# Performance work log

Hardware: AMD Instinct MI355X
Metric: run time of the kernel (lower is better)

The kernel has to match this reference:

```python
import jax, jax.numpy as jnp
import numpy as np

B, D, L, E, H = 8192, 1024, 256, 16, 400

def setup_inputs() -> dict:
    key = jax.random.key(0)
    ks = jax.random.split(key, 6)
    s1 = 1.0 / np.sqrt(D)
    s2 = 1.0 / np.sqrt(H)
    return {
        "x": jax.random.normal(ks[0], (B, D), dtype=jnp.float32),
        "angle_idx": jax.random.randint(ks[1], (B,), 0, E, dtype=jnp.int64),
        "W1": jax.random.uniform(ks[2], (E, D, H), jnp.float32, -s1, s1),
        "b1": jax.random.uniform(ks[3], (E, H), jnp.float32, -s1, s1),
        "W2": jax.random.uniform(ks[4], (E, H, 2 * L), jnp.float32, -s2, s2),
        "b2": jax.random.uniform(ks[5], (E, 2 * L), jnp.float32, -s2, s2),
    }

def reference(x, angle_idx, W1, b1, W2, b2):
    # Dense all-experts compute, then per-sample select (jit-friendly MoE dispatch).
    # h1: [E, B, H]
    h1 = jax.nn.relu(jnp.einsum('bd,edh->ebh', x, W1) + b1[:, None, :])
    # h: [E, B, 2L]
    h = jnp.einsum('ebh,ehk->ebk', h1, W2) + b2[:, None, :]
    sel = h[angle_idx, jnp.arange(x.shape[0])]  # [B, 2L], each row from its routed expert
    half = sel.shape[1] // 2
    z_mu, z_logvar = sel[:, :half], sel[:, half:]
    return (z_mu, z_logvar)
```

## Files before the change

kernel.cpp:

```cpp
#include <hip/hip_runtime.h>
#include <hip/hip_bf16.h>
#include <cstdint>
#include <cstddef>

#define B_N 8192
#define D_K 1024
#define H_N 400
#define HP  416
#define K2_N 512
#define E_N 16
#define L_N 256
#define TM 64
#define PAD_ROWS (B_N + E_N * TM)
#define NTILES (PAD_ROWS / TM)

typedef short bf16x8 __attribute__((ext_vector_type(8)));
typedef float f32x4 __attribute__((ext_vector_type(4)));

#define GLDS(gp, lp) __builtin_amdgcn_global_load_lds( \
    (const __attribute__((address_space(1))) unsigned int*)(gp), \
    (__attribute__((address_space(3))) unsigned int*)(lp), 16, 0, 0)

static __device__ __forceinline__ unsigned short f2bf(float f) {
  union { float f; unsigned int u; } c; c.f = f;
  unsigned int u = c.u + 0x7fffu + ((c.u >> 16) & 1u);
  return (unsigned short)(u >> 16);
}
static __device__ __forceinline__ unsigned int pkbf(float a, float b) {
  union { __hip_bfloat162 v; unsigned int u; } c;
  c.v = __float22bfloat162_rn(make_float2(a, b));
  return c.u;
}

__global__ __launch_bounds__(256) void prep_kernel(const float* __restrict__ W1,
                                                   const float* __restrict__ W2,
                                                   const int* __restrict__ idx,
                                                   unsigned short* __restrict__ Wt1,
                                                   unsigned short* __restrict__ Wt2,
                                                   int* __restrict__ off_al,
                                                   int* __restrict__ order) {
  const int bid = blockIdx.x;
  const int t = threadIdx.x;
  if (bid < 2688) {
    __shared__ unsigned short Ls[64][72];
    const float* S; unsigned short* Dt; int K, N, Kd, Nd, k0, n0;
    if (bid < 1792) {
      int e = bid / 112, r = bid % 112;
      k0 = (r % 16) * 64; n0 = (r / 16) * 64;
      S = W1 + (size_t)e * D_K * H_N; Dt = Wt1 + (size_t)e * HP * D_K;
      K = D_K; N = H_N; Kd = D_K; Nd = HP;
    } else {
      int t2 = bid - 1792; int e = t2 / 56, r = t2 % 56;
      k0 = (r % 7) * 64; n0 = (r / 7) * 64;
      S = W2 + (size_t)e * H_N * K2_N; Dt = Wt2 + (size_t)e * K2_N * HP;
      K = H_N; N = K2_N; Kd = HP; Nd = K2_N;
    }
    const int kk = t >> 4;
    const int nn = (t & 15) * 4;
#pragma unroll
    for (int p = 0; p < 4; ++p) {
      int k = k0 + p * 16 + kk;
      int n = n0 + nn;
      float4 v = make_float4(0.f, 0.f, 0.f, 0.f);
      if (k < K && n + 3 < N) v = *(const float4*)(S + (size_t)k * N + n);
      Ls[nn + 0][p * 16 + kk] = f2bf(v.x);
      Ls[nn + 1][p * 16 + kk] = f2bf(v.y);
      Ls[nn + 2][p * 16 + kk] = f2bf(v.z);
      Ls[nn + 3][p * 16 + kk] = f2bf(v.w);
    }
    __syncthreads();
    const int n2 = t >> 3;
    const int ch = t & 7;
#pragma unroll
    for (int p = 0; p < 2; ++p) {
      int n = n0 + p * 32 + n2;
      int k = k0 + ch * 8;
      if (n < Nd && k < Kd)
        *(uint4*)(Dt + (size_t)n * Kd + k) = *(const uint4*)&Ls[p * 32 + n2][ch * 8];
    }
  } else {
    __shared__ int cnt[E_N];
    __shared__ int curS[E_N];
    if (t < E_N) cnt[t] = 0;
    __syncthreads();
    for (int b = t; b < B_N; b += 256) atomicAdd(&cnt[idx[b]], 1);
    __syncthreads();
    if (t == 0) {
      int acc = 0;
      for (int e = 0; e < E_N; ++e) {
        off_al[e] = acc; curS[e] = acc;
        acc += ((cnt[e] + TM - 1) / TM) * TM;
      }
      off_al[E_N] = acc;
    }
    for (int i = t; i < PAD_ROWS; i += 256) order[i] = -1;
    __syncthreads();
    for (int b = t; b < B_N; b += 256) {
      int e = idx[b];
      order[atomicAdd(&curS[e], 1)] = b;
    }
  }
}

__global__ __launch_bounds__(256) void gather_x_kernel(const float* __restrict__ x,
                                                       const int* __restrict__ order,
                                                       unsigned short* __restrict__ xg) {
  const int w = threadIdx.x >> 6, l = threadIdx.x & 63;
  const int row = blockIdx.x * 4 + w;
  const int src = order[row];
  unsigned short* dst = xg + (size_t)row * D_K;
  if (src < 0) {
#pragma unroll
    for (int i = 0; i < 4; ++i)
      *(uint2*)(dst + i * 256 + l * 4) = make_uint2(0, 0);
  } else {
    const float* s = x + (size_t)src * D_K;
#pragma unroll
    for (int i = 0; i < 4; ++i) {
      float4 v = *(const float4*)(s + i * 256 + l * 4);
      uint2 o; o.x = pkbf(v.x, v.y); o.y = pkbf(v.z, v.w);
      *(uint2*)(dst + i * 256 + l * 4) = o;
    }
  }
}

__global__ __launch_bounds__(256) void gemm1_kernel(const unsigned short* __restrict__ xg,
                                                    const unsigned short* __restrict__ Wt1,
                                                    const float* __restrict__ b1,
                                                    const int* __restrict__ off_al,
                                                    unsigned short* __restrict__ h1buf) {
  __shared__ unsigned short As[2][64 * 32];
  __shared__ unsigned short Bs[2][112 * 32];
  __shared__ int offs[E_N + 1];
  const int tid = threadIdx.x;
  const int m0 = blockIdx.x * TM;
  const int nb = blockIdx.y;
  const int tstart = (nb < 2) ? 7 * nb : 14 + 6 * (nb - 2);
  const int tcnt   = (nb < 2) ? 7 : 6;
  if (tid <= E_N) offs[tid] = off_al[tid];
  __syncthreads();
  if (m0 >= offs[E_N]) return;
  int e = 0;
  while (m0 >= offs[e + 1]) ++e;
  const unsigned short* Wt1e = Wt1 + (size_t)e * HP * D_K;

  const int l = tid & 63, w = tid >> 6;
  const int r4 = l >> 2;
  const int sg = (r4 ^ (r4 >> 2)) & 3;
  const int g8 = ((l & 3) ^ sg) * 8;
  const int tl1 = w + 4;
  const unsigned short* gA  = xg + (size_t)(m0 + 16 * w + r4) * D_K + g8;
  const unsigned short* gB0 = Wt1e + (size_t)((tstart + w) * 16 + r4) * D_K + g8;
  const unsigned short* gB1 = Wt1e + (size_t)((tstart + tl1) * 16 + r4) * D_K + g8;

  const int ln = l & 15, q = l >> 4;
  const int sr = (ln ^ (ln >> 2)) & 3;
  const int cq = (q ^ sr) * 8;

  f32x4 acc[4][2] = {};

  GLDS(gA, &As[0][16 * w * 32]);
  GLDS(gB0, &Bs[0][16 * w * 32]);
  if (tl1 < tcnt) GLDS(gB1, &Bs[0][16 * tl1 * 32]);

  for (int k0 = 0; k0 < D_K; k0 += 32) {
    const int cur = (k0 >> 5) & 1;
    const int nxt = cur ^ 1;
    __syncthreads();
    if (k0 + 32 < D_K) {
      GLDS(gA + k0 + 32, &As[nxt][16 * w * 32]);
      GLDS(gB0 + k0 + 32, &Bs[nxt][16 * w * 32]);
      if (tl1 < tcnt) GLDS(gB1 + k0 + 32, &Bs[nxt][16 * tl1 * 32]);
    }
    bf16x8 af[4];
#pragma unroll
    for (int i = 0; i < 4; ++i)
      af[i] = *(const bf16x8*)&As[cur][(16 * i + ln) * 32 + cq];
    {
      bf16x8 bf0 = *(const bf16x8*)&Bs[cur][(16 * w + ln) * 32 + cq];
#pragma unroll
      for (int i = 0; i < 4; ++i)
        acc[i][0] = __builtin_amdgcn_mfma_f32_16x16x32_bf16(af[i], bf0, acc[i][0], 0, 0, 0);
    }
    if (tl1 < tcnt) {
      bf16x8 bf1 = *(const bf16x8*)&Bs[cur][(16 * tl1 + ln) * 32 + cq];
#pragma unroll
      for (int i = 0; i < 4; ++i)
        acc[i][1] = __builtin_amdgcn_mfma_f32_16x16x32_bf16(af[i], bf1, acc[i][1], 0, 0, 0);
    }
  }

#pragma unroll
  for (int t = 0; t < 2; ++t) {
    const int tl = w + 4 * t;
    if (tl < tcnt) {
      const int n = (tstart + tl) * 16 + ln;
      if (n < H_N) {
        const float bias = b1[e * H_N + n];
#pragma unroll
        for (int i = 0; i < 4; ++i)
#pragma unroll
          for (int r = 0; r < 4; ++r) {
            const int m = m0 + 16 * i + 4 * q + r;
            h1buf[(size_t)m * HP + n] = f2bf(fmaxf(acc[i][t][r] + bias, 0.f));
          }
      }
    }
  }
  if (nb == 3 && tid < TM) {
    uint4 z = make_uint4(0, 0, 0, 0);
    *(uint4*)&h1buf[(size_t)(m0 + tid) * HP + 400] = z;
    *(uint4*)&h1buf[(size_t)(m0 + tid) * HP + 408] = z;
  }
}

__global__ __launch_bounds__(256) void gemm2_kernel(const unsigned short* __restrict__ h1buf,
                                                    const unsigned short* __restrict__ Wt2,
                                                    const float* __restrict__ b2,
                                                    const int* __restrict__ off_al,
                                                    const int* __restrict__ order,
                                                    float* __restrict__ out) {
  __shared__ unsigned short As[2][64 * 32];
  __shared__ unsigned short Bs[2][128 * 32];
  __shared__ int offs[E_N + 1];
  __shared__ int rowidx[TM];
  const int tid = threadIdx.x;
  const int m0 = blockIdx.x * TM;
  const int nbase = blockIdx.y * 128;
  if (tid <= E_N) offs[tid] = off_al[tid];
  if (tid < TM) rowidx[tid] = order[m0 + tid];
  __syncthreads();
  if (m0 >= offs[E_N]) return;
  int e = 0;
  while (m0 >= offs[e + 1]) ++e;
  const unsigned short* Wt2e = Wt2 + (size_t)e * K2_N * HP;

  const int l = tid & 63, w = tid >> 6;
  const int r4 = l >> 2;
  const int sg = (r4 ^ (r4 >> 2)) & 3;
  const int g8 = ((l & 3) ^ sg) * 8;
  const int tl1 = w + 4;
  const unsigned short* gA  = h1buf + (size_t)(m0 + 16 * w + r4) * HP + g8;
  const unsigned short* gB0 = Wt2e + (size_t)(nbase + 16 * w + r4) * HP + g8;
  const unsigned short* gB1 = Wt2e + (size_t)(nbase + 16 * tl1 + r4) * HP + g8;

  const int ln = l & 15, q = l >> 4;
  const int sr = (ln ^ (ln >> 2)) & 3;
  const int cq = (q ^ sr) * 8;

  f32x4 acc[4][2] = {};

  GLDS(gA, &As[0][16 * w * 32]);
  GLDS(gB0, &Bs[0][16 * w * 32]);
  GLDS(gB1, &Bs[0][16 * tl1 * 32]);

  for (int k0 = 0; k0 < HP; k0 += 32) {
    const int cur = (k0 >> 5) & 1;
    const int nxt = cur ^ 1;
    __syncthreads();
    if (k0 + 32 < HP) {
      GLDS(gA + k0 + 32, &As[nxt][16 * w * 32]);
      GLDS(gB0 + k0 + 32, &Bs[nxt][16 * w * 32]);
      GLDS(gB1 + k0 + 32, &Bs[nxt][16 * tl1 * 32]);
    }
    bf16x8 af[4];
#pragma unroll
    for (int i = 0; i < 4; ++i)
      af[i] = *(const bf16x8*)&As[cur][(16 * i + ln) * 32 + cq];
#pragma unroll
    for (int t = 0; t < 2; ++t) {
      const int tl = w + 4 * t;
      bf16x8 bfr = *(const bf16x8*)&Bs[cur][(16 * tl + ln) * 32 + cq];
#pragma unroll
      for (int i = 0; i < 4; ++i)
        acc[i][t] = __builtin_amdgcn_mfma_f32_16x16x32_bf16(af[i], bfr, acc[i][t], 0, 0, 0);
    }
  }

#pragma unroll
  for (int t = 0; t < 2; ++t) {
    const int tl = w + 4 * t;
    const int n = nbase + 16 * tl + ln;
    const float bias = b2[e * K2_N + n];
#pragma unroll
    for (int i = 0; i < 4; ++i)
#pragma unroll
      for (int r = 0; r < 4; ++r) {
        const int s = rowidx[16 * i + 4 * q + r];
        if (s >= 0) {
          const float v = acc[i][t][r] + bias;
          if (n < L_N) out[(size_t)s * L_N + n] = v;
          else         out[(size_t)(B_N + s) * L_N + (n - L_N)] = v;
        }
      }
  }
}

extern "C" void kernel_launch(void* const* d_in, const int* in_sizes, int n_in,
                              void* d_out, int out_size, void* d_ws, size_t ws_size,
                              hipStream_t stream) {
  const float* x   = (const float*)d_in[0];
  const int*   idx = (const int*)d_in[1];
  const float* W1  = (const float*)d_in[2];
  const float* b1  = (const float*)d_in[3];
  const float* W2  = (const float*)d_in[4];
  const float* b2  = (const float*)d_in[5];
  float* out = (float*)d_out;

  char* ws = (char*)d_ws;
  int* off_al = (int*)(ws + 0);
  int* order  = (int*)(ws + 2240);
  unsigned short* xg  = (unsigned short*)(ws + 39104);
  unsigned short* h1  = (unsigned short*)(ws + 18913472);
  unsigned short* Wt1 = (unsigned short*)(ws + 26581184);
  unsigned short* Wt2 = (unsigned short*)(ws + 40212672);

  prep_kernel<<<2689, 256, 0, stream>>>(W1, W2, idx, Wt1, Wt2, off_al, order);
  gather_x_kernel<<<PAD_ROWS / 4, 256, 0, stream>>>(x, order, xg);
  gemm1_kernel<<<dim3(NTILES, 4), 256, 0, stream>>>(xg, Wt1, b1, off_al, h1);
  gemm2_kernel<<<dim3(NTILES, 4), 256, 0, stream>>>(h1, Wt2, b2, off_al, order, out);
}
```

Before: 179.3 us.

## Fold x bf16 conversion into prep kernel and gather rows inside GEMM1

Removes the separate gather_x kernel. The prep kernel now converts x to bf16 in its original row order and adds one zero row at the end. GEMM1 then gathers A rows indirectly through the order array, with padding rows pointing at the zero row. This drops a kernel launch and a full write and re-read of the permuted activation buffer. The cost is indirect, non-contiguous row addressing for the A loads in GEMM1.

Measured after the change: 175.4 us. 1.02x faster.

```diff
diff --git a/kernel.cpp b/kernel.cpp
--- a/kernel.cpp
+++ b/kernel.cpp
@@ -34,9 +34,11 @@
 
 __global__ __launch_bounds__(256) void prep_kernel(const float* __restrict__ W1,
                                                    const float* __restrict__ W2,
+                                                   const float* __restrict__ x,
                                                    const int* __restrict__ idx,
                                                    unsigned short* __restrict__ Wt1,
                                                    unsigned short* __restrict__ Wt2,
+                                                   unsigned short* __restrict__ xc,
                                                    int* __restrict__ off_al,
                                                    int* __restrict__ order) {
   const int bid = blockIdx.x;
@@ -78,9 +80,20 @@
       if (n < Nd && k < Kd)
         *(uint4*)(Dt + (size_t)n * Kd + k) = *(const uint4*)&Ls[p * 32 + n2][ch * 8];
     }
+  } else if (bid < 3200) {
+    const int xb = bid - 2688;
+    const float* S = x + (size_t)xb * 16 * D_K;
+    unsigned short* Dp = xc + (size_t)xb * 16 * D_K;
+#pragma unroll
+    for (int i = 0; i < 16; ++i) {
+      float4 v = *(const float4*)(S + i * D_K + t * 4);
+      uint2 o; o.x = pkbf(v.x, v.y); o.y = pkbf(v.z, v.w);
+      *(uint2*)(Dp + i * D_K + t * 4) = o;
+    }
   } else {
     __shared__ int cnt[E_N];
     __shared__ int curS[E_N];
+    *(uint2*)(xc + (size_t)B_N * D_K + t * 4) = make_uint2(0, 0);
     if (t < E_N) cnt[t] = 0;
     __syncthreads();
     for (int b = t; b < B_N; b += 256) atomicAdd(&cnt[idx[b]], 1);
@@ -102,42 +115,26 @@
   }
 }
 
-__global__ __launch_bounds__(256) void gather_x_kernel(const float* __restrict__ x,
-                                                       const int* __restrict__ order,
-                                                       unsigned short* __restrict__ xg) {
-  const int w = threadIdx.x >> 6, l = threadIdx.x & 63;
-  const int row = blockIdx.x * 4 + w;
-  const int src = order[row];
-  unsigned short* dst = xg + (size_t)row * D_K;
-  if (src < 0) {
-#pragma unroll
-    for (int i = 0; i < 4; ++i)
-      *(uint2*)(dst + i * 256 + l * 4) = make_uint2(0, 0);
-  } else {
-    const float* s = x + (size_t)src * D_K;
-#pragma unroll
-    for (int i = 0; i < 4; ++i) {
-      float4 v = *(const float4*)(s + i * 256 + l * 4);
-      uint2 o; o.x = pkbf(v.x, v.y); o.y = pkbf(v.z, v.w);
-      *(uint2*)(dst + i * 256 + l * 4) = o;
-    }
-  }
-}
-
-__global__ __launch_bounds__(256) void gemm1_kernel(const unsigned short* __restrict__ xg,
+__global__ __launch_bounds__(256) void gemm1_kernel(const unsigned short* __restrict__ xc,
                                                     const unsigned short* __restrict__ Wt1,
                                                     const float* __restrict__ b1,
                                                     const int* __restrict__ off_al,
+                                                    const int* __restrict__ order,
                                                     unsigned short* __restrict__ h1buf) {
   __shared__ unsigned short As[2][64 * 32];
   __shared__ unsigned short Bs[2][112 * 32];
   __shared__ int offs[E_N + 1];
+  __shared__ int rowidx[TM];
   const int tid = threadIdx.x;
   const int m0 = blockIdx.x * TM;
   const int nb = blockIdx.y;
   const int tstart = (nb < 2) ? 7 * nb : 14 + 6 * (nb - 2);
   const int tcnt   = (nb < 2) ? 7 : 6;
   if (tid <= E_N) offs[tid] = off_al[tid];
+  if (tid < TM) {
+    int s = order[m0 + tid];
+    rowidx[tid] = (s < 0) ? B_N : s;
+  }
   __syncthreads();
   if (m0 >= offs[E_N]) return;
   int e = 0;
@@ -149,7 +146,7 @@
   const int sg = (r4 ^ (r4 >> 2)) & 3;
   const int g8 = ((l & 3) ^ sg) * 8;
   const int tl1 = w + 4;
-  const unsigned short* gA  = xg + (size_t)(m0 + 16 * w + r4) * D_K + g8;
+  const unsigned short* gA  = xc + (size_t)rowidx[16 * w + r4] * D_K + g8;
   const unsigned short* gB0 = Wt1e + (size_t)((tstart + w) * 16 + r4) * D_K + g8;
   const unsigned short* gB1 = Wt1e + (size_t)((tstart + tl1) * 16 + r4) * D_K + g8;
 
@@ -310,13 +307,12 @@
   char* ws = (char*)d_ws;
   int* off_al = (int*)(ws + 0);
   int* order  = (int*)(ws + 2240);
-  unsigned short* xg  = (unsigned short*)(ws + 39104);
-  unsigned short* h1  = (unsigned short*)(ws + 18913472);
-  unsigned short* Wt1 = (unsigned short*)(ws + 26581184);
-  unsigned short* Wt2 = (unsigned short*)(ws + 40212672);
-
-  prep_kernel<<<2689, 256, 0, stream>>>(W1, W2, idx, Wt1, Wt2, off_al, order);
-  gather_x_kernel<<<PAD_ROWS / 4, 256, 0, stream>>>(x, order, xg);
-  gemm1_kernel<<<dim3(NTILES, 4), 256, 0, stream>>>(xg, Wt1, b1, off_al, h1);
+  unsigned short* xc  = (unsigned short*)(ws + 39104);
+  unsigned short* h1  = (unsigned short*)(ws + 16818368);
+  unsigned short* Wt1 = (unsigned short*)(ws + 24486080);
+  unsigned short* Wt2 = (unsigned short*)(ws + 38117568);
+
+  prep_kernel<<<3201, 256, 0, stream>>>(W1, W2, x, idx, Wt1, Wt2, xc, off_al, order);
+  gemm1_kernel<<<dim3(NTILES, 4), 256, 0, stream>>>(xc, Wt1, b1, off_al, order, h1);
   gemm2_kernel<<<dim3(NTILES, 4), 256, 0, stream>>>(h1, Wt2, b2, off_al, order, out);
 }
```
